# Optimization experiments

Hardware: AMD Instinct MI355X
Metric: run time of the kernel (lower is better)

## Reference

```python
import jax, jax.numpy as jnp
import numpy as np

N_NODES = 100000


def _gcn_norm(edge_index, num_nodes):
    # PyG GCNConv: add self-loops, symmetric normalization deg^-1/2 A deg^-1/2
    loops = jnp.arange(num_nodes, dtype=edge_index.dtype)
    src = jnp.concatenate([edge_index[0], loops])
    dst = jnp.concatenate([edge_index[1], loops])
    deg = jax.ops.segment_sum(jnp.ones_like(dst, dtype=jnp.float32), dst,
                              num_segments=num_nodes)
    dinv = jnp.where(deg > 0, jax.lax.rsqrt(deg), 0.0)
    norm = dinv[src] * dinv[dst]  # [E + N]
    return src, dst, norm


def _gcn_conv(x, src, dst, norm, W, b, num_nodes):
    h = x @ W                                   # [N, out]
    msg = h[src] * norm[:, None]                # gather + scale  [E+N, out]
    agg = jax.ops.segment_sum(msg, dst, num_segments=num_nodes)  # scatter-add
    return agg + b


def setup_inputs() -> dict:
    key = jax.random.key(0)
    k = jax.random.split(key, 8)
    nfeat, nhid, E = 256, 128, 1600000
    x = jax.random.normal(k[0], (N_NODES, nfeat), dtype=jnp.float32)
    edge_index = jax.random.randint(k[1], (2, E), 0, N_NODES, dtype=jnp.int32)
    # Glorot-style params (GCNConv weights + biases), Linear(nhid,1) xavier + zero bias
    s1 = float(np.sqrt(6.0 / (nfeat + nhid)))
    s2 = float(np.sqrt(6.0 / (nhid + nhid)))
    sf = float(np.sqrt(6.0 / (nhid + 1)))
    W1 = jax.random.uniform(k[2], (nfeat, nhid), jnp.float32, -s1, s1)
    b1 = jnp.zeros((nhid,), jnp.float32)
    W2 = jax.random.uniform(k[3], (nhid, nhid), jnp.float32, -s2, s2)
    b2 = jnp.zeros((nhid,), jnp.float32)
    Wf = jax.random.uniform(k[4], (nhid, 1), jnp.float32, -sf, sf)
    bf = jnp.zeros((1,), jnp.float32)
    return {"x": x, "edge_index": edge_index, "W1": W1, "b1": b1,
            "W2": W2, "b2": b2, "Wf": Wf, "bf": bf}


def reference(x, edge_index, W1, b1, W2, b2, Wf, bf):
    n = x.shape[0]
    src, dst, norm = _gcn_norm(edge_index, n)
    h = jax.nn.relu(_gcn_conv(x, src, dst, norm, W1, b1, n))
    # dropout is identity at inference
    h = _gcn_conv(h, src, dst, norm, W2, b2, n)
    out = h @ Wf + bf            # Linear(nhid, 1)
    return out.squeeze(-1)       # [N]
```

## Files before the change

### kernel.cpp

```cpp
#include <hip/hip_runtime.h>
#include <hip/hip_bf16.h>

#define NF 256
#define NH 128
#define PSZ_SH 7
#define MAXP 1024
#define NCB 512

typedef __attribute__((ext_vector_type(8))) short short8;
typedef __attribute__((ext_vector_type(4))) float float4v;

static __device__ __forceinline__ ushort f2bf(float f) {
  unsigned u = __float_as_uint(f);
  u = (u + 0x7fffu + ((u >> 16) & 1u)) >> 16;
  return (ushort)u;
}
static __device__ __forceinline__ float bflo(unsigned u) { return __uint_as_float(u << 16); }
static __device__ __forceinline__ float bfhi(unsigned u) { return __uint_as_float(u & 0xffff0000u); }

static __device__ __forceinline__ short8 pack_bf8(float4 v0, float4 v1) {
  short8 r;
  r[0] = (short)f2bf(v0.x); r[1] = (short)f2bf(v0.y);
  r[2] = (short)f2bf(v0.z); r[3] = (short)f2bf(v0.w);
  r[4] = (short)f2bf(v1.x); r[5] = (short)f2bf(v1.y);
  r[6] = (short)f2bf(v1.z); r[7] = (short)f2bf(v1.w);
  return r;
}

__global__ __launch_bounds__(256) void k_initall(
    const int* __restrict__ ei, int E, int P, int* __restrict__ bcnt, int chunk,
    const float* __restrict__ W1, ushort* __restrict__ Wfr,
    const float* __restrict__ W2, const float* __restrict__ Wfv,
    const float* __restrict__ b2, const float* __restrict__ bfv,
    float* __restrict__ Wc) {
  int b = blockIdx.x;
  if (b < 128) {
    int g = b * 256 + threadIdx.x;
    int ii   = g & 7;
    int lane = (g >> 3) & 63;
    int t    = (g >> 9) & 7;
    int ks   = g >> 12;
    int k = ks * 32 + ((lane >> 4) << 3) + ii;
    int c = t * 16 + (lane & 15);
    Wfr[g] = f2bf(W1[(size_t)k * NH + c]);
  } else if (b == 128) {
    __shared__ float wl[NH];
    if (threadIdx.x < NH) wl[threadIdx.x] = Wfv[threadIdx.x];
    __syncthreads();
    if (threadIdx.x < NH) {
      int i = threadIdx.x;
      const float4* w4 = reinterpret_cast<const float4*>(&W2[(size_t)i * NH]);
      float s = 0.f;
#pragma unroll 8
      for (int k = 0; k < NH / 4; ++k) {
        float4 v = w4[k];
        s += v.x * wl[4 * k] + v.y * wl[4 * k + 1] + v.z * wl[4 * k + 2] + v.w * wl[4 * k + 3];
      }
      Wc[i] = s;
      if (i == 0) {
        float c = 0.f;
        for (int k = 0; k < NH; ++k) c += b2[k] * wl[k];
        Wc[NH] = c + bfv[0];
      }
    }
  } else {
    int cb = b - 129;
    __shared__ int hc[MAXP];
    for (int j = threadIdx.x; j < P; j += 256) hc[j] = 0;
    __syncthreads();
    int start = cb * chunk;
    int endE = min(start + chunk, E);
    for (int e = start + (int)threadIdx.x; e < endE; e += 256)
      atomicAdd(&hc[ei[E + e] >> PSZ_SH], 1);
    __syncthreads();
    for (int j = threadIdx.x; j < P; j += 256) bcnt[cb * P + j] = hc[j];
  }
}

__global__ __launch_bounds__(NCB) void k_scanA(const int* __restrict__ bcnt,
                                               int* __restrict__ bloc,
                                               int* __restrict__ ptot, int P) {
  __shared__ int ws[NCB / 64];
  int p = blockIdx.x, tid = threadIdx.x, lane = tid & 63, wid = tid >> 6;
  int v = bcnt[tid * P + p];
  int pre = v;
#pragma unroll
  for (int m = 1; m < 64; m <<= 1) {
    int t = __shfl_up(pre, m, 64);
    if (lane >= m) pre += t;
  }
  if (lane == 63) ws[wid] = pre;
  __syncthreads();
  if (tid == 0) {
    int run = 0;
#pragma unroll
    for (int j = 0; j < NCB / 64; ++j) { int t = ws[j]; ws[j] = run; run += t; }
    ptot[p] = run;
  }
  __syncthreads();
  bloc[tid * P + p] = ws[wid] + pre - v;
}

__global__ __launch_bounds__(1024) void k_scanB(const int* __restrict__ ptot,
                                                int* __restrict__ pbase, int P, int E) {
  __shared__ int ws[16];
  int tid = threadIdx.x, lane = tid & 63, wid = tid >> 6;
  int v = (tid < P) ? ptot[tid] : 0;
  int pre = v;
#pragma unroll
  for (int m = 1; m < 64; m <<= 1) {
    int t = __shfl_up(pre, m, 64);
    if (lane >= m) pre += t;
  }
  if (lane == 63) ws[wid] = pre;
  __syncthreads();
  if (tid == 0) {
    int run = 0;
#pragma unroll
    for (int j = 0; j < 16; ++j) { int t = ws[j]; ws[j] = run; run += t; }
  }
  __syncthreads();
  if (tid < P) pbase[tid] = ws[wid] + pre - v;
  if (tid == 0) pbase[P] = E;
}

__global__ __launch_bounds__(256) void k_scatter(const int* __restrict__ ei, int E,
                                                 const int* __restrict__ pbase,
                                                 const int* __restrict__ bloc,
                                                 uint* __restrict__ sub, int chunk, int P) {
  __shared__ int cur[MAXP];
  int b = blockIdx.x;
  for (int j = threadIdx.x; j < P; j += 256) cur[j] = pbase[j] + bloc[b * P + j];
  __syncthreads();
  int start = b * chunk;
  int endE = min(start + chunk, E);
  for (int e = start + (int)threadIdx.x; e < endE; e += 256) {
    int s = ei[e];
    int d = ei[E + e];
    int pos = atomicAdd(&cur[d >> PSZ_SH], 1);
    sub[pos] = (uint)s | ((uint)(d & ((1 << PSZ_SH) - 1)) << 20);
  }
}

__global__ __launch_bounds__(256) void k_bucket(const uint* __restrict__ sub,
                                                const int* __restrict__ pbase,
                                                int* __restrict__ rowptr, int* __restrict__ deg,
                                                float* __restrict__ dinv, int* __restrict__ csr,
                                                int N) {
  __shared__ int hist[1 << PSZ_SH];
  __shared__ int curL[1 << PSZ_SH];
  __shared__ int wsum[2];
  const int p = blockIdx.x, tid = threadIdx.x;
  const int base = pbase[p];
  const int cnt = pbase[p + 1] - base;
  const int node0 = p << PSZ_SH;
  if (tid < (1 << PSZ_SH)) hist[tid] = 0;
  __syncthreads();
  for (int e = tid; e < cnt; e += 256) atomicAdd(&hist[sub[base + e] >> 20], 1);
  __syncthreads();
  int d = 0, pre = 0;
  if (tid < (1 << PSZ_SH)) {
    d = hist[tid];
    pre = d;
#pragma unroll
    for (int m = 1; m < 64; m <<= 1) {
      int t = __shfl_up(pre, m, 64);
      if ((tid & 63) >= m) pre += t;
    }
    if ((tid & 63) == 63) wsum[tid >> 6] = pre;
  }
  __syncthreads();
  if (tid < (1 << PSZ_SH)) {
    int excl = base + ((tid >= 64) ? wsum[0] : 0) + pre - d;
    curL[tid] = excl;
    int node = node0 + tid;
    if (node < N) {
      rowptr[node] = excl;
      deg[node] = d;
      dinv[node] = rsqrtf((float)d + 1.0f);
    }
  }
  __syncthreads();
  for (int e = tid; e < cnt; e += 256) {
    uint v = sub[base + e];
    int pos = atomicAdd(&curL[v >> 20], 1);
    csr[pos] = (int)(v & 0xFFFFFu);
  }
}

__global__ __launch_bounds__(256, 2) void k_gemm1(
    const float* __restrict__ x, const ushort* __restrict__ Wf,
    const float* __restrict__ dinv, ushort* __restrict__ hs, int N) {
  __shared__ ushort Ol[64][136];
  const int tid = threadIdx.x;
  const int w = tid >> 6, l = tid & 63;
  const int row0 = blockIdx.x * 64;
  const int arow = row0 + 16 * w + (l & 15);
  const int kg = l >> 4;
  const bool rv = arow < N;
  const float* xr = &x[(size_t)(rv ? arow : 0) * NF + kg * 8];

  float4 xf0[8], xf1[8];
#pragma unroll
  for (int ks = 0; ks < 8; ++ks) {
    xf0[ks] = *reinterpret_cast<const float4*>(&xr[ks * 32]);
    xf1[ks] = *reinterpret_cast<const float4*>(&xr[ks * 32 + 4]);
  }
  __builtin_amdgcn_sched_barrier(0);

  short8 afr[8];
#pragma unroll
  for (int ks = 0; ks < 8; ++ks) {
    float4 v0 = xf0[ks], v1 = xf1[ks];
    if (!rv) { v0 = make_float4(0.f, 0.f, 0.f, 0.f); v1 = v0; }
    afr[ks] = pack_bf8(v0, v1);
  }

  const short8* Wb = reinterpret_cast<const short8*>(Wf);
  float4v acc[8];
#pragma unroll
  for (int t = 0; t < 8; ++t) acc[t] = (float4v){0.f, 0.f, 0.f, 0.f};
  short8 bc[8], bn[8];
#pragma unroll
  for (int ks = 0; ks < 8; ++ks) bc[ks] = Wb[(ks * 8 + 0) * 64 + l];
#pragma unroll
  for (int tp = 0; tp < 4; ++tp) {
    const int t0 = 2 * tp, t1 = 2 * tp + 1;
#pragma unroll
    for (int ks = 0; ks < 8; ++ks) bn[ks] = Wb[(ks * 8 + t1) * 64 + l];
    __builtin_amdgcn_sched_barrier(0);
#pragma unroll
    for (int ks = 0; ks < 8; ++ks)
      acc[t0] = __builtin_amdgcn_mfma_f32_16x16x32_bf16(afr[ks], bc[ks], acc[t0], 0, 0, 0);
    if (tp < 3) {
#pragma unroll
      for (int ks = 0; ks < 8; ++ks) bc[ks] = Wb[(ks * 8 + t1 + 1) * 64 + l];
      __builtin_amdgcn_sched_barrier(0);
    }
#pragma unroll
    for (int ks = 0; ks < 8; ++ks)
      acc[t1] = __builtin_amdgcn_mfma_f32_16x16x32_bf16(afr[ks], bn[ks], acc[t1], 0, 0, 0);
  }

  float dj[4];
#pragma unroll
  for (int j = 0; j < 4; ++j) {
    int grow = row0 + 16 * w + (l >> 4) * 4 + j;
    dj[j] = (grow < N) ? dinv[grow] : 0.f;
  }
#pragma unroll
  for (int t = 0; t < 8; ++t)
#pragma unroll
    for (int j = 0; j < 4; ++j)
      Ol[16 * w + (l >> 4) * 4 + j][16 * t + (l & 15)] = f2bf(acc[t][j] * dj[j]);
  __syncthreads();
  {
    const int r = tid >> 2, grow = row0 + r;
    if (grow < N) {
      uint* dsts = (uint*)hs;
#pragma unroll
      for (int q = 0; q < 4; ++q) {
        uint4 v = *reinterpret_cast<const uint4*>(&Ol[r][(tid & 3) * 32 + q * 8]);
        *reinterpret_cast<uint4*>(&dsts[(size_t)grow * 64 + (tid & 3) * 16 + q * 4]) = v;
      }
    }
  }
}

static __device__ __forceinline__ void accg(float2* a, uint4 u) {
  a[0].x += __uint_as_float(u.x << 16); a[0].y += __uint_as_float(u.x);
  a[1].x += __uint_as_float(u.y << 16); a[1].y += __uint_as_float(u.y);
  a[2].x += __uint_as_float(u.z << 16); a[2].y += __uint_as_float(u.z);
  a[3].x += __uint_as_float(u.w << 16); a[3].y += __uint_as_float(u.w);
}

__global__ __launch_bounds__(256) void k_agg1_z(
    const uint4* __restrict__ hs4, const int* __restrict__ rowptr,
    const int* __restrict__ deg, const int* __restrict__ csr,
    const float* __restrict__ dinv, const float* __restrict__ b1,
    const float* __restrict__ Wc, float* __restrict__ zs,
    float* __restrict__ out, int N) {
  int g = blockIdx.x * blockDim.x + threadIdx.x;
  int i = g >> 6;
  if (i >= N) return;
  int lane = threadIdx.x & 63;
  int q = lane >> 4;
  int sub = lane & 15;

  float2 a2[4];
  {
    uint4 u = hs4[(size_t)i * 16 + sub];
    if (q) { u.x = 0u; u.y = 0u; u.z = 0u; u.w = 0u; }
    a2[0] = make_float2(bflo(u.x), bfhi(u.x));
    a2[1] = make_float2(bflo(u.y), bfhi(u.y));
    a2[2] = make_float2(bflo(u.z), bfhi(u.z));
    a2[3] = make_float2(bflo(u.w), bfhi(u.w));
  }

  int kk = rowptr[i];
  const int end = kk + deg[i];
  for (; kk + 15 < end; kk += 16) {
    int c0 = csr[kk + q];
    int c1 = csr[kk + 4 + q];
    int c2 = csr[kk + 8 + q];
    int c3 = csr[kk + 12 + q];
    uint4 u0 = hs4[(size_t)c0 * 16 + sub];
    uint4 u1 = hs4[(size_t)c1 * 16 + sub];
    uint4 u2 = hs4[(size_t)c2 * 16 + sub];
    uint4 u3 = hs4[(size_t)c3 * 16 + sub];
    accg(a2, u0); accg(a2, u1); accg(a2, u2); accg(a2, u3);
  }
  for (; kk + 3 < end; kk += 4) {
    int c = csr[kk + q];
    uint4 u = hs4[(size_t)c * 16 + sub];
    accg(a2, u);
  }
  int r = end - kk;
  if (r > 0) {
    int c = csr[kk + (q < r ? q : r - 1)];
    uint4 u = hs4[(size_t)c * 16 + sub];
    if (q >= r) { u.x = 0u; u.y = 0u; u.z = 0u; u.w = 0u; }
    accg(a2, u);
  }

  float a[8] = {a2[0].x, a2[0].y, a2[1].x, a2[1].y, a2[2].x, a2[2].y, a2[3].x, a2[3].y};
#pragma unroll
  for (int j = 0; j < 8; ++j) {
    a[j] += __shfl_xor(a[j], 16, 64);
    a[j] += __shfl_xor(a[j], 32, 64);
  }

  float d = dinv[i];
  float4 ba = reinterpret_cast<const float4*>(b1)[2 * sub];
  float4 bb = reinterpret_cast<const float4*>(b1)[2 * sub + 1];
  float4 wa = reinterpret_cast<const float4*>(Wc)[2 * sub];
  float4 wb = reinterpret_cast<const float4*>(Wc)[2 * sub + 1];
  float s = fmaxf(fmaf(d, a[0], ba.x), 0.f) * wa.x
          + fmaxf(fmaf(d, a[1], ba.y), 0.f) * wa.y
          + fmaxf(fmaf(d, a[2], ba.z), 0.f) * wa.z
          + fmaxf(fmaf(d, a[3], ba.w), 0.f) * wa.w
          + fmaxf(fmaf(d, a[4], bb.x), 0.f) * wb.x
          + fmaxf(fmaf(d, a[5], bb.y), 0.f) * wb.y
          + fmaxf(fmaf(d, a[6], bb.z), 0.f) * wb.z
          + fmaxf(fmaf(d, a[7], bb.w), 0.f) * wb.w;
#pragma unroll
  for (int m = 8; m >= 1; m >>= 1) s += __shfl_xor(s, m, 64);
  if (lane == 0) {
    float zsv = d * s;
    zs[i] = zsv;
    out[i] = d * zsv + Wc[NH];
  }
}

__global__ void k_out2(const int* __restrict__ rowptr, const int* __restrict__ deg,
                       const int* __restrict__ csr, const float* __restrict__ zs,
                       const float* __restrict__ dinv, float* __restrict__ out, int N) {
  int i = blockIdx.x * blockDim.x + threadIdx.x;
  if (i >= N) return;
  int k = rowptr[i], end = k + deg[i];
  float s = 0.f;
  for (; k + 3 < end; k += 4) {
    float t0 = zs[csr[k]], t1 = zs[csr[k + 1]], t2 = zs[csr[k + 2]], t3 = zs[csr[k + 3]];
    s += (t0 + t1) + (t2 + t3);
  }
  for (; k < end; ++k) s += zs[csr[k]];
  out[i] += dinv[i] * s;
}

extern "C" void kernel_launch(void* const* d_in, const int* in_sizes, int n_in,
                              void* d_out, int out_size, void* d_ws, size_t ws_size,
                              hipStream_t stream) {
  const float* x  = (const float*)d_in[0];
  const int*   ei = (const int*)d_in[1];
  const float* W1 = (const float*)d_in[2];
  const float* b1 = (const float*)d_in[3];
  const float* W2 = (const float*)d_in[4];
  const float* b2 = (const float*)d_in[5];
  const float* Wf = (const float*)d_in[6];
  const float* bf = (const float*)d_in[7];
  const int N = in_sizes[0] / NF;
  const int E = in_sizes[1] / 2;
  const int P = (N + (1 << PSZ_SH) - 1) >> PSZ_SH;
  const int chunk = (E + NCB - 1) / NCB;

  char* ws = (char*)d_ws;
  size_t off = 0;
  auto alloc = [&](size_t bytes) {
    void* p = ws + off;
    off = (off + bytes + 255) & ~(size_t)255;
    return p;
  };
  ushort* hs     = (ushort*)alloc((size_t)N * NH * 2);
  ushort* Wfrag  = (ushort*)alloc((size_t)NF * NH * 2);
  int*    csr    = (int*)alloc((size_t)E * 4);
  uint*   sub    = (uint*)alloc((size_t)E * 4);
  int*    deg    = (int*)alloc((size_t)N * 4);
  int*    rowptr = (int*)alloc((size_t)N * 4);
  float*  dinv   = (float*)alloc((size_t)N * 4);
  float*  zs     = (float*)alloc((size_t)N * 4);
  float*  Wc     = (float*)alloc(132 * 4);
  int*    bcnt   = (int*)alloc((size_t)NCB * P * 4);
  int*    bloc   = (int*)alloc((size_t)NCB * P * 4);
  int*    ptot   = (int*)alloc((size_t)P * 4);
  int*    pbase  = (int*)alloc((size_t)(P + 1) * 4);
  float*  out    = (float*)d_out;

  const int b = 256;
  k_initall<<<129 + NCB, b, 0, stream>>>(ei, E, P, bcnt, chunk,
                                         W1, Wfrag, W2, Wf, b2, bf, Wc);
  k_scanA  <<<P, NCB, 0, stream>>>(bcnt, bloc, ptot, P);
  k_scanB  <<<1, 1024, 0, stream>>>(ptot, pbase, P, E);
  k_scatter<<<NCB, b, 0, stream>>>(ei, E, pbase, bloc, sub, chunk, P);
  k_bucket <<<P, b, 0, stream>>>(sub, pbase, rowptr, deg, dinv, csr, N);
  k_gemm1  <<<(N + 63) / 64, 256, 0, stream>>>(x, Wfrag, dinv, hs, N);
  k_agg1_z <<<(int)(((size_t)N * 64 + b - 1) / b), b, 0, stream>>>(
      (const uint4*)hs, rowptr, deg, csr, dinv, b1, Wc, zs, out, N);
  k_out2   <<<(N + b - 1) / b, b, 0, stream>>>(rowptr, deg, csr, zs, dinv, out, N);
}
```

Measured before the change: 159.1 us.

## Split hidden features into four column slabs for cache-resident aggregation passes

The GEMM output is stored as four separate feature slabs of 32 columns each, one per quarter of the hidden dimension, instead of interleaved rows. Aggregation runs as four passes, each gathering only one slab, so the working set per pass (about 6.4MB) is more likely to stay in L2/LLC during random neighbor gathers. The per-slab partial dot products with the folded output weights are summed by a new combine kernel. In exchange, CSR indices are re-read four times, each gather fetches only 4 bytes per lane, and extra launches are added.

```diff
diff --git a/kernel.cpp b/kernel.cpp
--- a/kernel.cpp
+++ b/kernel.cpp
@@ -190,7 +190,7 @@
 
 __global__ __launch_bounds__(256, 2) void k_gemm1(
     const float* __restrict__ x, const ushort* __restrict__ Wf,
-    const float* __restrict__ dinv, ushort* __restrict__ hs, int N) {
+    const float* __restrict__ dinv, uint* __restrict__ hs, int N) {
   __shared__ ushort Ol[64][136];
   const int tid = threadIdx.x;
   const int w = tid >> 6, l = tid & 63;
@@ -256,30 +256,23 @@
   __syncthreads();
   {
     const int r = tid >> 2, grow = row0 + r;
+    const int qt = tid & 3;
     if (grow < N) {
-      uint* dsts = (uint*)hs;
-#pragma unroll
-      for (int q = 0; q < 4; ++q) {
-        uint4 v = *reinterpret_cast<const uint4*>(&Ol[r][(tid & 3) * 32 + q * 8]);
-        *reinterpret_cast<uint4*>(&dsts[(size_t)grow * 64 + (tid & 3) * 16 + q * 4]) = v;
+      uint* dstq = hs + (size_t)qt * N * 16 + (size_t)grow * 16;
+#pragma unroll
+      for (int q2 = 0; q2 < 4; ++q2) {
+        uint4 v = *reinterpret_cast<const uint4*>(&Ol[r][qt * 32 + q2 * 8]);
+        *reinterpret_cast<uint4*>(&dstq[q2 * 4]) = v;
       }
     }
   }
 }
 
-static __device__ __forceinline__ void accg(float2* a, uint4 u) {
-  a[0].x += __uint_as_float(u.x << 16); a[0].y += __uint_as_float(u.x);
-  a[1].x += __uint_as_float(u.y << 16); a[1].y += __uint_as_float(u.y);
-  a[2].x += __uint_as_float(u.z << 16); a[2].y += __uint_as_float(u.z);
-  a[3].x += __uint_as_float(u.w << 16); a[3].y += __uint_as_float(u.w);
-}
-
-__global__ __launch_bounds__(256) void k_agg1_z(
-    const uint4* __restrict__ hs4, const int* __restrict__ rowptr,
+__global__ __launch_bounds__(256) void k_aggq(
+    const uint* __restrict__ hq, const int* __restrict__ rowptr,
     const int* __restrict__ deg, const int* __restrict__ csr,
-    const float* __restrict__ dinv, const float* __restrict__ b1,
-    const float* __restrict__ Wc, float* __restrict__ zs,
-    float* __restrict__ out, int N) {
+    const float* __restrict__ dinv, const float* __restrict__ b1q,
+    const float* __restrict__ Wcq, float* __restrict__ zp, int N) {
   int g = blockIdx.x * blockDim.x + threadIdx.x;
   int i = g >> 6;
   if (i >= N) return;
@@ -287,14 +280,11 @@
   int q = lane >> 4;
   int sub = lane & 15;
 
-  float2 a2[4];
+  float ax, ay;
   {
-    uint4 u = hs4[(size_t)i * 16 + sub];
-    if (q) { u.x = 0u; u.y = 0u; u.z = 0u; u.w = 0u; }
-    a2[0] = make_float2(bflo(u.x), bfhi(u.x));
-    a2[1] = make_float2(bflo(u.y), bfhi(u.y));
-    a2[2] = make_float2(bflo(u.z), bfhi(u.z));
-    a2[3] = make_float2(bflo(u.w), bfhi(u.w));
+    uint u = hq[(size_t)i * 16 + sub];
+    if (q) u = 0u;
+    ax = bflo(u); ay = bfhi(u);
   }
 
   int kk = rowptr[i];
@@ -304,52 +294,51 @@
     int c1 = csr[kk + 4 + q];
     int c2 = csr[kk + 8 + q];
     int c3 = csr[kk + 12 + q];
-    uint4 u0 = hs4[(size_t)c0 * 16 + sub];
-    uint4 u1 = hs4[(size_t)c1 * 16 + sub];
-    uint4 u2 = hs4[(size_t)c2 * 16 + sub];
-    uint4 u3 = hs4[(size_t)c3 * 16 + sub];
-    accg(a2, u0); accg(a2, u1); accg(a2, u2); accg(a2, u3);
+    uint u0 = hq[(size_t)c0 * 16 + sub];
+    uint u1 = hq[(size_t)c1 * 16 + sub];
+    uint u2 = hq[(size_t)c2 * 16 + sub];
+    uint u3 = hq[(size_t)c3 * 16 + sub];
+    ax += bflo(u0); ay += __uint_as_float(u0);
+    ax += bflo(u1); ay += __uint_as_float(u1);
+    ax += bflo(u2); ay += __uint_as_float(u2);
+    ax += bflo(u3); ay += __uint_as_float(u3);
   }
   for (; kk + 3 < end; kk += 4) {
     int c = csr[kk + q];
-    uint4 u = hs4[(size_t)c * 16 + sub];
-    accg(a2, u);
+    uint u = hq[(size_t)c * 16 + sub];
+    ax += bflo(u); ay += __uint_as_float(u);
   }
   int r = end - kk;
   if (r > 0) {
     int c = csr[kk + (q < r ? q : r - 1)];
-    uint4 u = hs4[(size_t)c * 16 + sub];
-    if (q >= r) { u.x = 0u; u.y = 0u; u.z = 0u; u.w = 0u; }
-    accg(a2, u);
-  }
-
-  float a[8] = {a2[0].x, a2[0].y, a2[1].x, a2[1].y, a2[2].x, a2[2].y, a2[3].x, a2[3].y};
-#pragma unroll
-  for (int j = 0; j < 8; ++j) {
-    a[j] += __shfl_xor(a[j], 16, 64);
-    a[j] += __shfl_xor(a[j], 32, 64);
-  }
+    uint u = hq[(size_t)c * 16 + sub];
+    if (q >= r) u = 0u;
+    ax += bflo(u); ay += __uint_as_float(u);
+  }
+
+  ax += __shfl_xor(ax, 16, 64); ax += __shfl_xor(ax, 32, 64);
+  ay += __shfl_xor(ay, 16, 64); ay += __shfl_xor(ay, 32, 64);
 
   float d = dinv[i];
-  float4 ba = reinterpret_cast<const float4*>(b1)[2 * sub];
-  float4 bb = reinterpret_cast<const float4*>(b1)[2 * sub + 1];
-  float4 wa = reinterpret_cast<const float4*>(Wc)[2 * sub];
-  float4 wb = reinterpret_cast<const float4*>(Wc)[2 * sub + 1];
-  float s = fmaxf(fmaf(d, a[0], ba.x), 0.f) * wa.x
-          + fmaxf(fmaf(d, a[1], ba.y), 0.f) * wa.y
-          + fmaxf(fmaf(d, a[2], ba.z), 0.f) * wa.z
-          + fmaxf(fmaf(d, a[3], ba.w), 0.f) * wa.w
-          + fmaxf(fmaf(d, a[4], bb.x), 0.f) * wb.x
-          + fmaxf(fmaf(d, a[5], bb.y), 0.f) * wb.y
-          + fmaxf(fmaf(d, a[6], bb.z), 0.f) * wb.z
-          + fmaxf(fmaf(d, a[7], bb.w), 0.f) * wb.w;
+  float2 bb = reinterpret_cast<const float2*>(b1q)[sub];
+  float2 ww = reinterpret_cast<const float2*>(Wcq)[sub];
+  float s = fmaxf(fmaf(d, ax, bb.x), 0.f) * ww.x
+          + fmaxf(fmaf(d, ay, bb.y), 0.f) * ww.y;
 #pragma unroll
   for (int m = 8; m >= 1; m >>= 1) s += __shfl_xor(s, m, 64);
-  if (lane == 0) {
-    float zsv = d * s;
-    zs[i] = zsv;
-    out[i] = d * zsv + Wc[NH];
-  }
+  if (lane == 0) zp[i] = s;
+}
+
+__global__ void k_zcomb(const float* __restrict__ zp, const float* __restrict__ dinv,
+                        const float* __restrict__ Wc, float* __restrict__ zs,
+                        float* __restrict__ out, int N) {
+  int i = blockIdx.x * blockDim.x + threadIdx.x;
+  if (i >= N) return;
+  float z = (zp[i] + zp[(size_t)N + i]) + (zp[(size_t)2 * N + i] + zp[(size_t)3 * N + i]);
+  float d = dinv[i];
+  float zsv = d * z;
+  zs[i] = zsv;
+  out[i] = d * zsv + Wc[NH];
 }
 
 __global__ void k_out2(const int* __restrict__ rowptr, const int* __restrict__ deg,
@@ -390,7 +379,7 @@
     off = (off + bytes + 255) & ~(size_t)255;
     return p;
   };
-  ushort* hs     = (ushort*)alloc((size_t)N * NH * 2);
+  uint*   hs     = (uint*)alloc((size_t)N * NH * 2);
   ushort* Wfrag  = (ushort*)alloc((size_t)NF * NH * 2);
   int*    csr    = (int*)alloc((size_t)E * 4);
   uint*   sub    = (uint*)alloc((size_t)E * 4);
@@ -398,6 +387,7 @@
   int*    rowptr = (int*)alloc((size_t)N * 4);
   float*  dinv   = (float*)alloc((size_t)N * 4);
   float*  zs     = (float*)alloc((size_t)N * 4);
+  float*  zp     = (float*)alloc((size_t)N * 4 * 4);
   float*  Wc     = (float*)alloc(132 * 4);
   int*    bcnt   = (int*)alloc((size_t)NCB * P * 4);
   int*    bloc   = (int*)alloc((size_t)NCB * P * 4);
@@ -413,7 +403,12 @@
   k_scatter<<<NCB, b, 0, stream>>>(ei, E, pbase, bloc, sub, chunk, P);
   k_bucket <<<P, b, 0, stream>>>(sub, pbase, rowptr, deg, dinv, csr, N);
   k_gemm1  <<<(N + 63) / 64, 256, 0, stream>>>(x, Wfrag, dinv, hs, N);
-  k_agg1_z <<<(int)(((size_t)N * 64 + b - 1) / b), b, 0, stream>>>(
-      (const uint4*)hs, rowptr, deg, csr, dinv, b1, Wc, zs, out, N);
+  const int aggGrid = (int)(((size_t)N * 64 + b - 1) / b);
+  for (int p4 = 0; p4 < 4; ++p4) {
+    k_aggq <<<aggGrid, b, 0, stream>>>(hs + (size_t)p4 * N * 16, rowptr, deg, csr,
+                                       dinv, b1 + p4 * 32, Wc + p4 * 32,
+                                       zp + (size_t)p4 * N, N);
+  }
+  k_zcomb  <<<(N + b - 1) / b, b, 0, stream>>>(zp, dinv, Wc, zs, out, N);
   k_out2   <<<(N + b - 1) / b, b, 0, stream>>>(rowptr, deg, csr, zs, dinv, out, N);
 }
```

Result: slower. 273.6 us (+71.9%).
